# Performance work log

Measured on AMD Instinct MI355X. Metric: run time of the kernel, lower is better.

## Reference

```python
import jax, jax.numpy as jnp
import numpy as np

B, S1, S2 = 32, 60, 60
H, L, D = 100, 20, 300
V, CLS = 30000, 3


def _lstm(x, Wih, Whh, bih, bhh):
    # x: (B,T,Din); PyTorch gate order i,f,g,o
    xp = jnp.einsum('btd,gd->btg', x, Wih) + bih  # (B,T,4H)
    Hh = Whh.shape[1]
    init = (jnp.zeros((x.shape[0], Hh), x.dtype), jnp.zeros((x.shape[0], Hh), x.dtype))
    def step(carry, xt):
        hprev, cprev = carry
        g = xt + hprev @ Whh.T + bhh
        i, f, gg, o = jnp.split(g, 4, axis=-1)
        c = jax.nn.sigmoid(f) * cprev + jax.nn.sigmoid(i) * jnp.tanh(gg)
        hh = jax.nn.sigmoid(o) * jnp.tanh(c)
        return (hh, c), hh
    (hT, _), hs = jax.lax.scan(step, init, jnp.swapaxes(xp, 0, 1))
    return jnp.swapaxes(hs, 0, 1), hT


def _bilstm(x, pf, pb):
    hs_f, hT_f = _lstm(x, *pf)
    hs_b, hT_b = _lstm(x[:, ::-1], *pb)
    return hs_f, hs_b[:, ::-1], hT_f, hT_b


def _mp_single(v1, u, w):
    # cosine(w*v1_i, w*u) per perspective; v1 (B,S,H), u (B,H), w (H,L) -> (B,L,S)
    w2 = w * w
    n1 = jnp.sqrt(jnp.einsum('bih,hl->bil', v1 * v1, w2))
    nu = jnp.sqrt(jnp.einsum('bh,hl->bl', u * u, w2))
    num = jnp.einsum('bih,hl,bh->bil', v1, w2, u)
    return jnp.swapaxes(num / (n1 * nu[:, None, :]), 1, 2)


def _mp_pairwise(v1, v2, w):
    # full (B,L,S1,S2) multi-perspective cosine without materializing (B,L,S,H)
    w2 = w * w
    n1 = jnp.sqrt(jnp.einsum('bih,hl->bil', v1 * v1, w2))  # (B,S1,L)
    n2 = jnp.sqrt(jnp.einsum('bjh,hl->bjl', v2 * v2, w2))  # (B,S2,L)
    num = jnp.einsum('bih,hl,bjh->blij', v1, w2, v2)
    return num / (jnp.moveaxis(n1, 2, 1)[..., None] * jnp.moveaxis(n2, 2, 1)[:, :, None, :])


def _cos_attn(v1, v2):
    n1 = jnp.linalg.norm(v1, axis=2, keepdims=True)
    n2 = jnp.linalg.norm(v2, axis=2, keepdims=True)
    return jnp.einsum('bih,bjh->bij', v1, v2) / (n1 * jnp.swapaxes(n2, 1, 2))


def _match_dir(cp, ch, w_full, w_max, w_am, w_amax, last_idx):
    mv_p_full = _mp_single(cp, ch[:, last_idx], w_full)
    mv_h_full = _mp_single(ch, cp[:, last_idx], w_full)
    m = _mp_pairwise(cp, ch, w_max)
    mv_p_max = m.max(axis=3)
    mv_h_max = m.max(axis=2)
    a = _cos_attn(cp, ch)  # (B,S1,S2)
    mean_h = jnp.einsum('bij,bjh->bih', a, ch) / (a.sum(2, keepdims=True) + 1e-10)
    mean_p = jnp.einsum('bij,bih->bjh', a, cp) / (a.sum(1)[..., None] + 1e-10)
    max_h = (ch[:, None, :, :] * a[..., None]).max(axis=2)  # (B,S1,H)
    max_p = (cp[:, :, None, :] * a[..., None]).max(axis=1)  # (B,S2,H)
    # original code slices [:, :, :, 0] -> matches against v2 position 0
    mv_p_am = _mp_single(cp, mean_h[:, 0], w_am)
    mv_h_am = _mp_single(ch, mean_p[:, 0], w_am)
    mv_p_amax = _mp_single(cp, max_h[:, 0], w_amax)
    mv_h_amax = _mp_single(ch, max_p[:, 0], w_amax)
    return (mv_p_full, mv_p_max, mv_p_am, mv_p_amax), (mv_h_full, mv_h_max, mv_h_am, mv_h_amax)


def _forward(p_idx, h_idx, word_emb, ctxf, ctxb, ws, aggf, aggb, fc1_W, fc1_b, fc2_W, fc2_b):
    p = word_emb[p_idx]
    h = word_emb[h_idx]
    cpf, cpb, _, _ = _bilstm(p, ctxf, ctxb)
    chf, chb, _, _ = _bilstm(h, ctxf, ctxb)
    w1, w2, w3, w4, w5, w6, w7, w8 = ws
    pf, hf = _match_dir(cpf, chf, w1, w3, w5, w7, -1)
    pb, hb = _match_dir(cpb, chb, w2, w4, w6, w8, 0)
    mv_p = jnp.swapaxes(jnp.concatenate(pf + pb, axis=1), 1, 2)  # (B,S1,8L)
    mv_h = jnp.swapaxes(jnp.concatenate(hf + hb, axis=1), 1, 2)
    _, _, pTf, pTb = _bilstm(mv_p, aggf, aggb)
    _, _, hTf, hTb = _bilstm(mv_h, aggf, aggb)
    x = jnp.concatenate([pTf, pTb, hTf, hTb], axis=1)  # (B,4H)
    x = jnp.tanh(x @ fc1_W.T + fc1_b)
    return x @ fc2_W.T + fc2_b


def setup_inputs() -> dict:
    key = jax.random.key(0)
    ks = iter(jax.random.split(key, 48))
    def nrm(shape, s):
        return (jax.random.normal(next(ks), shape) * s).astype(jnp.float32)
    inp = {}
    inp['p'] = jax.random.randint(next(ks), (B, S1), 0, V)
    inp['h'] = jax.random.randint(next(ks), (B, S2), 0, V)
    inp['word_emb'] = nrm((V, D), 0.1)
    for pre, din in (('ctx', D), ('agg', 8 * L)):
        for d in ('f', 'b'):
            inp[pre + '_Wih_' + d] = nrm((4 * H, din), (2.0 / din) ** 0.5)
            inp[pre + '_Whh_' + d] = nrm((4 * H, H), (1.0 / H) ** 0.5)
            inp[pre + '_bih_' + d] = jnp.zeros((4 * H,), jnp.float32)
            inp[pre + '_bhh_' + d] = jnp.zeros((4 * H,), jnp.float32)
    for i in range(1, 9):
        inp['w' + str(i)] = nrm((H, L), (2.0 / H) ** 0.5)
    inp['fc1_W'] = nrm((2 * H, 4 * H), 0.005)
    inp['fc1_b'] = jnp.zeros((2 * H,), jnp.float32)
    inp['fc2_W'] = nrm((CLS, 2 * H), 0.005)
    inp['fc2_b'] = jnp.zeros((CLS,), jnp.float32)
    return inp


def reference(p, h, word_emb, ctx_Wih_f, ctx_Whh_f, ctx_bih_f, ctx_bhh_f, ctx_Wih_b, ctx_Whh_b, ctx_bih_b, ctx_bhh_b, w1, w2, w3, w4, w5, w6, w7, w8, agg_Wih_f, agg_Whh_f, agg_bih_f, agg_bhh_f, agg_Wih_b, agg_Whh_b, agg_bih_b, agg_bhh_b, fc1_W, fc1_b, fc2_W, fc2_b):
    return _forward(p, h, word_emb,
                    (ctx_Wih_f, ctx_Whh_f, ctx_bih_f, ctx_bhh_f),
                    (ctx_Wih_b, ctx_Whh_b, ctx_bih_b, ctx_bhh_b),
                    (w1, w2, w3, w4, w5, w6, w7, w8),
                    (agg_Wih_f, agg_Whh_f, agg_bih_f, agg_bhh_f),
                    (agg_Wih_b, agg_Whh_b, agg_bih_b, agg_bhh_b),
                    fc1_W, fc1_b, fc2_W, fc2_b)
```

## Files before the change

kernel.cpp:

```cpp
#include <hip/hip_runtime.h>
#include <math.h>

#define B_   32
#define T_   60
#define D_   300
#define HID  100
#define G4   400
#define L_   20

#define XP_OFF   0u
#define HSC_OFF  3072000u
#define HSA_OFF  3840000u
#define MV_OFF   4608000u
#define AV_OFF   5222400u

__global__ __launch_bounds__(256) void gemm_dual(
    const float* __restrict__ A0, const float* __restrict__ A1,
    const int* __restrict__ idx0, const int* __restrict__ idx1,
    const float* __restrict__ Wf, const float* __restrict__ Wb,
    const float* __restrict__ bf, const float* __restrict__ bb,
    float* __restrict__ C, int K)
{
    __shared__ float As[16][68];
    __shared__ float Bs[16][68];
    const int tid = threadIdx.x;
    const int m0 = blockIdx.y * 64;
    const int n0 = blockIdx.x * 64;
    const bool is_h = (m0 >= 1920);
    const float* __restrict__ Abase = is_h ? A1 : A0;
    const int* __restrict__ idx = is_h ? idx1 : idx0;
    const int mloc0 = m0 - (is_h ? 1920 : 0);

    const int r = tid >> 2;
    const int q = tid & 3;

    const int arow = mloc0 + r;
    const int srow = idx ? idx[arow] : arow;
    const float* __restrict__ Arow = Abase + (size_t)srow * K;
    const int n_my = n0 + r;
    const float* __restrict__ Wrow = (n_my < 400) ? (Wf + (size_t)n_my * K)
                      : ((n_my < 800) ? (Wb + (size_t)(n_my - 400) * K) : nullptr);

    const int tm = (tid >> 4) << 2;
    const int tn = (tid & 15) << 2;
    float acc[4][4] = {};
    for (int k0 = 0; k0 < K; k0 += 16) {
        const int k = k0 + q * 4;
        float4 av4 = make_float4(0.f, 0.f, 0.f, 0.f);
        float4 bv4 = make_float4(0.f, 0.f, 0.f, 0.f);
        if (k < K) av4 = *reinterpret_cast<const float4*>(Arow + k);
        if (Wrow != nullptr && k < K) bv4 = *reinterpret_cast<const float4*>(Wrow + k);
        __syncthreads();
        As[q * 4 + 0][r] = av4.x; As[q * 4 + 1][r] = av4.y;
        As[q * 4 + 2][r] = av4.z; As[q * 4 + 3][r] = av4.w;
        Bs[q * 4 + 0][r] = bv4.x; Bs[q * 4 + 1][r] = bv4.y;
        Bs[q * 4 + 2][r] = bv4.z; Bs[q * 4 + 3][r] = bv4.w;
        __syncthreads();
        #pragma unroll
        for (int kk = 0; kk < 16; ++kk) {
            const float4 a4 = *reinterpret_cast<const float4*>(&As[kk][tm]);
            const float4 b4 = *reinterpret_cast<const float4*>(&Bs[kk][tn]);
            const float a[4] = {a4.x, a4.y, a4.z, a4.w};
            const float b[4] = {b4.x, b4.y, b4.z, b4.w};
            #pragma unroll
            for (int i = 0; i < 4; i++)
                #pragma unroll
                for (int j = 0; j < 4; j++) acc[i][j] = fmaf(a[i], b[j], acc[i][j]);
        }
    }
    #pragma unroll
    for (int i = 0; i < 4; i++)
        #pragma unroll
        for (int j = 0; j < 4; j++) {
            const int n = n0 + tn + j;
            if (n < 800) {
                const int m = m0 + tm + i;
                const int s = (m >= 1920 ? 2 : 0) + (n >= 400 ? 1 : 0);
                const int ml = m - (m >= 1920 ? 1920 : 0);
                const int nl = n - (n >= 400 ? 400 : 0);
                const float bias = (n >= 400) ? bb[nl] : bf[nl];
                C[((size_t)s * 1920 + ml) * 400 + nl] = acc[i][j] + bias;
            }
        }
}

__global__ __launch_bounds__(512, 1) void lstm_scan(
    const float* __restrict__ xp,
    const float* __restrict__ Whh_f, const float* __restrict__ Whh_b,
    const float* __restrict__ bhh_f, const float* __restrict__ bhh_b,
    float* __restrict__ hs)
{
    const int blk = blockIdx.x;
    const int s = blk >> 5, b = blk & 31;
    const int dir = s & 1;
    const float* __restrict__ Whh = dir ? Whh_b : Whh_f;
    const float* __restrict__ bhh = dir ? bhh_b : bhh_f;
    const int tid = threadIdx.x;

    __shared__ __align__(16) float h_lds[HID];
    __shared__ float gact[G4];

    float wreg[HID];
    float bias = 0.f;
    if (tid < G4) {
        bias = bhh[tid];
        #pragma unroll
        for (int k = 0; k < HID; ++k) wreg[k] = Whh[tid * HID + k];
    }
    if (tid < HID) h_lds[tid] = 0.f;
    float c_reg = 0.f;

    const float* __restrict__ xp0 = xp + ((size_t)s * B_ + b) * T_ * G4;
    float* __restrict__ hs0 = hs + ((size_t)s * B_ + b) * T_ * HID;

    int t = dir ? (T_ - 1) : 0;
    const int tstep = dir ? -1 : 1;
    float xr = (tid < G4) ? xp0[(size_t)t * G4 + tid] : 0.f;
    __syncthreads();

    for (int st = 0; st < T_; ++st) {
        const int tcur = t;
        if (tid < G4) {
            float a0 = bias + xr, a1 = 0.f, a2 = 0.f, a3 = 0.f;
            #pragma unroll
            for (int k = 0; k < HID; k += 4) {
                const float4 h4 = *reinterpret_cast<const float4*>(&h_lds[k]);
                a0 = fmaf(h4.x, wreg[k + 0], a0);
                a1 = fmaf(h4.y, wreg[k + 1], a1);
                a2 = fmaf(h4.z, wreg[k + 2], a2);
                a3 = fmaf(h4.w, wreg[k + 3], a3);
            }
            if (st + 1 < T_) xr = xp0[(size_t)(t + tstep) * G4 + tid];
            const float acc = (a0 + a1) + (a2 + a3);
            const int chunk = tid / HID;
            float av;
            if (chunk == 2) av = tanhf(acc);
            else av = 1.f / (1.f + expf(-acc));
            gact[tid] = av;
        }
        __syncthreads();
        if (tid < HID) {
            const float iv = gact[tid], fv = gact[HID + tid];
            const float gv = gact[2 * HID + tid], ov = gact[3 * HID + tid];
            c_reg = fv * c_reg + iv * gv;
            const float hv = ov * tanhf(c_reg);
            h_lds[tid] = hv;
            hs0[(size_t)tcur * HID + tid] = hv;
        }
        t += tstep;
        __syncthreads();
    }
}

__global__ __launch_bounds__(128) void attn_kernel(
    const float* __restrict__ hs_ctx, float* __restrict__ av)
{
    const int d = blockIdx.x >> 5;
    const int b = blockIdx.x & 31;
    const float* __restrict__ cp = hs_ctx + ((size_t)(0 + d) * B_ + b) * T_ * HID;
    const float* __restrict__ ch = hs_ctx + ((size_t)(2 + d) * B_ + b) * T_ * HID;
    const int tid = threadIdx.x;
    __shared__ float cp0[HID], ch0[HID];
    __shared__ float arow[T_], acol[T_];
    __shared__ float nrm[2], asum[2];
    if (tid < HID) { cp0[tid] = cp[tid]; ch0[tid] = ch[tid]; }
    __syncthreads();
    if (tid < 2) {
        const float* v = tid ? ch0 : cp0;
        float sum = 0.f;
        for (int h = 0; h < HID; h++) sum += v[h] * v[h];
        nrm[tid] = sqrtf(sum);
    }
    __syncthreads();
    if (tid < T_) {
        const float* r = ch + (size_t)tid * HID;
        float dot = 0.f, n2 = 0.f;
        for (int h = 0; h < HID; h++) { const float x = r[h]; dot += cp0[h] * x; n2 += x * x; }
        arow[tid] = dot / (nrm[0] * sqrtf(n2));
    } else if (tid >= 64 && tid < 64 + T_) {
        const int i = tid - 64;
        const float* r = cp + (size_t)i * HID;
        float dot = 0.f, n2 = 0.f;
        for (int h = 0; h < HID; h++) { const float x = r[h]; dot += x * ch0[h]; n2 += x * x; }
        acol[i] = dot / (sqrtf(n2) * nrm[1]);
    }
    __syncthreads();
    if (tid < 2) {
        const float* a = tid ? acol : arow;
        float sum = 0.f;
        for (int j = 0; j < T_; j++) sum += a[j];
        asum[tid] = sum;
    }
    __syncthreads();
    if (tid < HID) {
        float m = 0.f, mx = -INFINITY;
        for (int j = 0; j < T_; j++) {
            const float x = ch[(size_t)j * HID + tid] * arow[j];
            m += x; mx = fmaxf(mx, x);
        }
        av[((size_t)(d * 4 + 0) * B_ + b) * HID + tid] = m / (asum[0] + 1e-10f);
        av[((size_t)(d * 4 + 1) * B_ + b) * HID + tid] = mx;
        float m2 = 0.f, mx2 = -INFINITY;
        for (int i = 0; i < T_; i++) {
            const float x = cp[(size_t)i * HID + tid] * acol[i];
            m2 += x; mx2 = fmaxf(mx2, x);
        }
        av[((size_t)(d * 4 + 2) * B_ + b) * HID + tid] = m2 / (asum[1] + 1e-10f);
        av[((size_t)(d * 4 + 3) * B_ + b) * HID + tid] = mx2;
    }
}

struct MPCfg {
    const float* v1;
    const float* u;
    int ustride;
    const float* w;
    float* outp;
    int choff;
};
struct MPCfgs { MPCfg c[12]; };

__global__ __launch_bounds__(256) void mp_single_kernel(MPCfgs cfgs)
{
    const int ci = blockIdx.x >> 5;
    const int b = blockIdx.x & 31;
    const MPCfg cfg = cfgs.c[ci];
    const int tid = threadIdx.x;
    __shared__ float w2[HID][L_];
    __shared__ float uw[HID][L_];
    __shared__ float u_l[HID];
    __shared__ float nul[L_];
    if (tid < HID) u_l[tid] = cfg.u[(size_t)b * cfg.ustride + tid];
    for (int e = tid; e < HID * L_; e += 256) {
        const float wv = cfg.w[e];
        w2[e / L_][e % L_] = wv * wv;
    }
    __syncthreads();
    for (int e = tid; e < HID * L_; e += 256) uw[e / L_][e % L_] = w2[e / L_][e % L_] * u_l[e / L_];
    if (tid < L_) {
        float sum = 0.f;
        for (int h = 0; h < HID; h++) sum += u_l[h] * u_l[h] * w2[h][tid];
        nul[tid] = sqrtf(sum);
    }
    __syncthreads();
    const float* __restrict__ v1b = cfg.v1 + (size_t)b * T_ * HID;
    for (int p = tid; p < T_ * L_; p += 256) {
        const int i = p / L_, l = p % L_;
        const float* __restrict__ v = v1b + (size_t)i * HID;
        float num = 0.f, den = 0.f;
        for (int h = 0; h < HID; h++) {
            const float x = v[h];
            num = fmaf(x, uw[h][l], num);
            den = fmaf(x * x, w2[h][l], den);
        }
        cfg.outp[((size_t)b * T_ + i) * 160 + cfg.choff + l] = num / (sqrtf(den) * nul[l]);
    }
}

__global__ __launch_bounds__(256) void mp_pair_kernel(
    const float* __restrict__ hs_ctx, const float* __restrict__ w3,
    const float* __restrict__ w4, float* __restrict__ mv_p, float* __restrict__ mv_h)
{
    const int x = blockIdx.x;
    const int l = x % L_;
    const int b = (x / L_) & 31;
    const int d = x / (L_ * B_);
    const float* __restrict__ cp = hs_ctx + ((size_t)(0 + d) * B_ + b) * T_ * HID;
    const float* __restrict__ ch = hs_ctx + ((size_t)(2 + d) * B_ + b) * T_ * HID;
    const float* __restrict__ w = d ? w4 : w3;
    const int tid = threadIdx.x;

    __shared__ __align__(16) float Ut[HID][T_];
    __shared__ __align__(16) float Vt[HID][T_];
    __shared__ float aw[HID];
    __shared__ float rn1[T_], rn2[T_];
    float* pmi = &Ut[0][0];
    float* pmj = &Ut[0][0] + 60 * 17 + 4;

    if (tid < HID) aw[tid] = fabsf(w[tid * L_ + l]);
    __syncthreads();
    for (int e = tid; e < T_ * HID; e += 256) {
        const int i = e / HID, h = e % HID;
        const float a = aw[h];
        Ut[h][i] = cp[e] * a;
        Vt[h][i] = ch[e] * a;
    }
    __syncthreads();
    if (tid < T_) {
        float s = 0.f;
        for (int h = 0; h < HID; h++) { const float v = Ut[h][tid]; s = fmaf(v, v, s); }
        rn1[tid] = 1.0f / sqrtf(s);
    } else if (tid >= 64 && tid < 64 + T_) {
        const int j = tid - 64;
        float s = 0.f;
        for (int h = 0; h < HID; h++) { const float v = Vt[h][j]; s = fmaf(v, v, s); }
        rn2[j] = 1.0f / sqrtf(s);
    }
    __syncthreads();

    float rmax[4], cmax[4];
    int i0 = 0, j0 = 0, ti = 0, tj = 0;
    if (tid < 225) {
        tj = tid % 15;
        ti = tid / 15;
        i0 = tj * 4; j0 = ti * 4;
        float acc[4][4] = {};
        #pragma unroll 4
        for (int h = 0; h < HID; ++h) {
            const float4 u = *reinterpret_cast<const float4*>(&Ut[h][i0]);
            const float4 v = *reinterpret_cast<const float4*>(&Vt[h][j0]);
            const float uu[4] = {u.x, u.y, u.z, u.w};
            const float vv[4] = {v.x, v.y, v.z, v.w};
            #pragma unroll
            for (int r2 = 0; r2 < 4; r2++)
                #pragma unroll
                for (int s2 = 0; s2 < 4; s2++) acc[r2][s2] = fmaf(uu[r2], vv[s2], acc[r2][s2]);
        }
        const float r1[4] = {rn1[i0], rn1[i0 + 1], rn1[i0 + 2], rn1[i0 + 3]};
        const float r2v[4] = {rn2[j0], rn2[j0 + 1], rn2[j0 + 2], rn2[j0 + 3]};
        #pragma unroll
        for (int r2 = 0; r2 < 4; r2++) { rmax[r2] = -INFINITY; }
        #pragma unroll
        for (int s2 = 0; s2 < 4; s2++) { cmax[s2] = -INFINITY; }
        #pragma unroll
        for (int r2 = 0; r2 < 4; r2++)
            #pragma unroll
            for (int s2 = 0; s2 < 4; s2++) {
                const float val = acc[r2][s2] * (r1[r2] * r2v[s2]);
                rmax[r2] = fmaxf(rmax[r2], val);
                cmax[s2] = fmaxf(cmax[s2], val);
            }
    }
    __syncthreads();
    if (tid < 225) {
        #pragma unroll
        for (int r2 = 0; r2 < 4; r2++) pmi[(i0 + r2) * 17 + ti] = rmax[r2];
        #pragma unroll
        for (int s2 = 0; s2 < 4; s2++) pmj[tj * 61 + (j0 + s2)] = cmax[s2];
    }
    __syncthreads();
    if (tid < T_) {
        float mx = -INFINITY;
        for (int q = 0; q < 15; q++) mx = fmaxf(mx, pmi[tid * 17 + q]);
        mv_p[((size_t)b * T_ + tid) * 160 + d * 80 + 20 + l] = mx;
    } else if (tid >= 64 && tid < 64 + T_) {
        const int j = tid - 64;
        float mx = -INFINITY;
        for (int q = 0; q < 15; q++) mx = fmaxf(mx, pmj[q * 61 + j]);
        mv_h[((size_t)b * T_ + j) * 160 + d * 80 + 20 + l] = mx;
    }
}

__global__ __launch_bounds__(256) void fc_final(
    const float* __restrict__ hs_agg, const float* __restrict__ fc1W,
    const float* __restrict__ fc1b, const float* __restrict__ fc2W,
    const float* __restrict__ fc2b, float* __restrict__ out)
{
    const int b = blockIdx.x;
    const int tid = threadIdx.x;
    __shared__ float x[400];
    __shared__ float y[200];
    if (tid < HID) {
        x[tid]           = hs_agg[((size_t)(0 * B_ + b) * T_ + 59) * HID + tid];
        x[HID + tid]     = hs_agg[((size_t)(1 * B_ + b) * T_ + 0) * HID + tid];
        x[2 * HID + tid] = hs_agg[((size_t)(2 * B_ + b) * T_ + 59) * HID + tid];
        x[3 * HID + tid] = hs_agg[((size_t)(3 * B_ + b) * T_ + 0) * HID + tid];
    }
    __syncthreads();
    if (tid < 200) {
        float s = fc1b[tid];
        const float* __restrict__ wr = fc1W + (size_t)tid * 400;
        for (int k = 0; k < 400; k++) s = fmaf(x[k], wr[k], s);
        y[tid] = tanhf(s);
    }
    __syncthreads();
    if (tid < 3) {
        float s = fc2b[tid];
        const float* __restrict__ wr = fc2W + (size_t)tid * 200;
        for (int k = 0; k < 200; k++) s = fmaf(y[k], wr[k], s);
        out[b * 3 + tid] = s;
    }
}

extern "C" void kernel_launch(void* const* d_in, const int* in_sizes, int n_in,
                              void* d_out, int out_size, void* d_ws, size_t ws_size,
                              hipStream_t stream) {
    const int* p_idx = (const int*)d_in[0];
    const int* h_idx = (const int*)d_in[1];
    const float* emb = (const float*)d_in[2];
    const float* ctx_Wih_f = (const float*)d_in[3];
    const float* ctx_Whh_f = (const float*)d_in[4];
    const float* ctx_bih_f = (const float*)d_in[5];
    const float* ctx_bhh_f = (const float*)d_in[6];
    const float* ctx_Wih_b = (const float*)d_in[7];
    const float* ctx_Whh_b = (const float*)d_in[8];
    const float* ctx_bih_b = (const float*)d_in[9];
    const float* ctx_bhh_b = (const float*)d_in[10];
    const float* agg_Wih_f = (const float*)d_in[11];
    const float* agg_Whh_f = (const float*)d_in[12];
    const float* agg_bih_f = (const float*)d_in[13];
    const float* agg_bhh_f = (const float*)d_in[14];
    const float* agg_Wih_b = (const float*)d_in[15];
    const float* agg_Whh_b = (const float*)d_in[16];
    const float* agg_bih_b = (const float*)d_in[17];
    const float* agg_bhh_b = (const float*)d_in[18];
    const float* w1 = (const float*)d_in[19];
    const float* w2 = (const float*)d_in[20];
    const float* w3 = (const float*)d_in[21];
    const float* w4 = (const float*)d_in[22];
    const float* w5 = (const float*)d_in[23];
    const float* w6 = (const float*)d_in[24];
    const float* w7 = (const float*)d_in[25];
    const float* w8 = (const float*)d_in[26];
    const float* fc1W = (const float*)d_in[27];
    const float* fc1b = (const float*)d_in[28];
    const float* fc2W = (const float*)d_in[29];
    const float* fc2b = (const float*)d_in[30];

    float* ws = (float*)d_ws;
    float* xp = ws + XP_OFF;
    float* hsc = ws + HSC_OFF;
    float* hsa = ws + HSA_OFF;
    float* mvp = ws + MV_OFF;
    float* mvh = mvp + (size_t)B_ * T_ * 160;
    float* av = ws + AV_OFF;

    const dim3 ggrid(13, 60);

    gemm_dual<<<ggrid, 256, 0, stream>>>(emb, emb, p_idx, h_idx,
                                         ctx_Wih_f, ctx_Wih_b, ctx_bih_f, ctx_bih_b, xp, 300);

    lstm_scan<<<128, 512, 0, stream>>>(xp, ctx_Whh_f, ctx_Whh_b, ctx_bhh_f, ctx_bhh_b, hsc);

    attn_kernel<<<64, 128, 0, stream>>>(hsc, av);

    MPCfgs cfgs;
    for (int d = 0; d < 2; d++) {
        const float* cp_d = hsc + (size_t)(0 + d) * B_ * T_ * HID;
        const float* ch_d = hsc + (size_t)(2 + d) * B_ * T_ * HID;
        const int last = d ? 0 : (T_ - 1);
        const float* wfull = d ? w2 : w1;
        const float* wam = d ? w6 : w5;
        const float* wamax = d ? w8 : w7;
        float* avp0 = av + (size_t)(d * 4 + 0) * B_ * HID;
        float* avp1 = av + (size_t)(d * 4 + 1) * B_ * HID;
        float* avp2 = av + (size_t)(d * 4 + 2) * B_ * HID;
        float* avp3 = av + (size_t)(d * 4 + 3) * B_ * HID;
        cfgs.c[d * 6 + 0] = {cp_d, ch_d + last * HID, T_ * HID, wfull, mvp, d * 80 + 0};
        cfgs.c[d * 6 + 1] = {cp_d, avp0, HID, wam, mvp, d * 80 + 40};
        cfgs.c[d * 6 + 2] = {cp_d, avp1, HID, wamax, mvp, d * 80 + 60};
        cfgs.c[d * 6 + 3] = {ch_d, cp_d + last * HID, T_ * HID, wfull, mvh, d * 80 + 0};
        cfgs.c[d * 6 + 4] = {ch_d, avp2, HID, wam, mvh, d * 80 + 40};
        cfgs.c[d * 6 + 5] = {ch_d, avp3, HID, wamax, mvh, d * 80 + 60};
    }
    mp_single_kernel<<<384, 256, 0, stream>>>(cfgs);
    mp_pair_kernel<<<1280, 256, 0, stream>>>(hsc, w3, w4, mvp, mvh);

    gemm_dual<<<ggrid, 256, 0, stream>>>(mvp, mvh, nullptr, nullptr,
                                         agg_Wih_f, agg_Wih_b, agg_bih_f, agg_bih_b, xp, 160);

    lstm_scan<<<128, 512, 0, stream>>>(xp, agg_Whh_f, agg_Whh_b, agg_bhh_f, agg_bhh_b, hsa);

    fc_final<<<32, 256, 0, stream>>>(hsa, fc1W, fc1b, fc2W, fc2b, (float*)d_out);
}
```

Measured before the change: 360.6 us.

## Interleave LSTM gates per hidden unit and combine via shuffles, one barrier per step

The input-projection GEMM now writes gate outputs interleaved so the four gates of each hidden unit sit in adjacent lanes. The scan kernel assigns each hidden unit a quad of threads that exchange activations with xor shuffles instead of a shared gate buffer. A double-buffered hidden state removes one of the two barriers per timestep. It also uses a single exp-based activation for both sigmoid and tanh, prefetches the input two steps ahead, and shrinks the block to 448 threads. This cuts per-step synchronisation and LDS traffic on the serial recurrence critical path, at the cost of tighter coupling between the GEMM output layout and the scan.

```diff
diff --git a/kernel.cpp b/kernel.cpp
--- a/kernel.cpp
+++ b/kernel.cpp
@@ -79,12 +79,13 @@
                 const int ml = m - (m >= 1920 ? 1920 : 0);
                 const int nl = n - (n >= 400 ? 400 : 0);
                 const float bias = (n >= 400) ? bb[nl] : bf[nl];
-                C[((size_t)s * 1920 + ml) * 400 + nl] = acc[i][j] + bias;
+                const int pos = (nl % 100) * 4 + nl / 100;
+                C[((size_t)s * 1920 + ml) * 400 + pos] = acc[i][j] + bias;
             }
         }
 }
 
-__global__ __launch_bounds__(512, 1) void lstm_scan(
+__global__ __launch_bounds__(448, 1) void lstm_scan(
     const float* __restrict__ xp,
     const float* __restrict__ Whh_f, const float* __restrict__ Whh_b,
     const float* __restrict__ bhh_f, const float* __restrict__ bhh_b,
@@ -96,18 +97,21 @@
     const float* __restrict__ Whh = dir ? Whh_b : Whh_f;
     const float* __restrict__ bhh = dir ? bhh_b : bhh_f;
     const int tid = threadIdx.x;
-
-    __shared__ __align__(16) float h_lds[HID];
-    __shared__ float gact[G4];
+    const int g = tid & 3;
+    const int j = tid >> 2;
+    const bool act = tid < G4;
+
+    __shared__ __align__(16) float h_lds[2][HID];
 
     float wreg[HID];
     float bias = 0.f;
-    if (tid < G4) {
-        bias = bhh[tid];
-        #pragma unroll
-        for (int k = 0; k < HID; ++k) wreg[k] = Whh[tid * HID + k];
-    }
-    if (tid < HID) h_lds[tid] = 0.f;
+    if (act) {
+        const int row = g * HID + j;
+        bias = bhh[row];
+        #pragma unroll
+        for (int k = 0; k < HID; ++k) wreg[k] = Whh[row * HID + k];
+    }
+    if (tid < HID) h_lds[0][tid] = 0.f;
     float c_reg = 0.f;
 
     const float* __restrict__ xp0 = xp + ((size_t)s * B_ + b) * T_ * G4;
@@ -115,39 +119,44 @@
 
     int t = dir ? (T_ - 1) : 0;
     const int tstep = dir ? -1 : 1;
-    float xr = (tid < G4) ? xp0[(size_t)t * G4 + tid] : 0.f;
+    float xA = 0.f, xB = 0.f;
+    if (act) {
+        xA = xp0[(size_t)t * G4 + tid];
+        xB = xp0[(size_t)(t + tstep) * G4 + tid];
+    }
+    int cur = 0;
     __syncthreads();
 
     for (int st = 0; st < T_; ++st) {
-        const int tcur = t;
-        if (tid < G4) {
-            float a0 = bias + xr, a1 = 0.f, a2 = 0.f, a3 = 0.f;
+        if (act) {
+            const float4* __restrict__ hp = reinterpret_cast<const float4*>(h_lds[cur]);
+            float a0 = bias + xA, a1 = 0.f, a2 = 0.f, a3 = 0.f;
             #pragma unroll
             for (int k = 0; k < HID; k += 4) {
-                const float4 h4 = *reinterpret_cast<const float4*>(&h_lds[k]);
+                const float4 h4 = hp[k >> 2];
                 a0 = fmaf(h4.x, wreg[k + 0], a0);
                 a1 = fmaf(h4.y, wreg[k + 1], a1);
                 a2 = fmaf(h4.z, wreg[k + 2], a2);
                 a3 = fmaf(h4.w, wreg[k + 3], a3);
             }
-            if (st + 1 < T_) xr = xp0[(size_t)(t + tstep) * G4 + tid];
+            xA = xB;
+            if (st + 2 < T_) xB = xp0[(size_t)(t + 2 * tstep) * G4 + tid];
             const float acc = (a0 + a1) + (a2 + a3);
-            const int chunk = tid / HID;
-            float av;
-            if (chunk == 2) av = tanhf(acc);
-            else av = 1.f / (1.f + expf(-acc));
-            gact[tid] = av;
-        }
-        __syncthreads();
-        if (tid < HID) {
-            const float iv = gact[tid], fv = gact[HID + tid];
-            const float gv = gact[2 * HID + tid], ov = gact[3 * HID + tid];
-            c_reg = fv * c_reg + iv * gv;
-            const float hv = ov * tanhf(c_reg);
-            h_lds[tid] = hv;
-            hs0[(size_t)tcur * HID + tid] = hv;
+            const float z = (g == 2) ? (-2.f * acc) : (-acc);
+            const float sig = 1.f / (1.f + expf(z));
+            const float a = (g == 2) ? fmaf(2.f, sig, -1.f) : sig;
+            const float v1 = __shfl_xor(a, 1);
+            const float v2 = __shfl_xor(a, 2);
+            const float v3 = __shfl_xor(v1, 2);
+            if (g == 0) {
+                c_reg = fmaf(v1, c_reg, a * v2);
+                const float hv = v3 * tanhf(c_reg);
+                h_lds[cur ^ 1][j] = hv;
+                hs0[(size_t)t * HID + j] = hv;
+            }
         }
         t += tstep;
+        cur ^= 1;
         __syncthreads();
     }
 }
@@ -430,7 +439,7 @@
     gemm_dual<<<ggrid, 256, 0, stream>>>(emb, emb, p_idx, h_idx,
                                          ctx_Wih_f, ctx_Wih_b, ctx_bih_f, ctx_bih_b, xp, 300);
 
-    lstm_scan<<<128, 512, 0, stream>>>(xp, ctx_Whh_f, ctx_Whh_b, ctx_bhh_f, ctx_bhh_b, hsc);
+    lstm_scan<<<128, 448, 0, stream>>>(xp, ctx_Whh_f, ctx_Whh_b, ctx_bhh_f, ctx_bhh_b, hsc);
 
     attn_kernel<<<64, 128, 0, stream>>>(hsc, av);
 
@@ -459,7 +468,7 @@
     gemm_dual<<<ggrid, 256, 0, stream>>>(mvp, mvh, nullptr, nullptr,
                                          agg_Wih_f, agg_Wih_b, agg_bih_f, agg_bih_b, xp, 160);
 
-    lstm_scan<<<128, 512, 0, stream>>>(xp, agg_Whh_f, agg_Whh_b, agg_bhh_f, agg_bhh_b, hsa);
+    lstm_scan<<<128, 448, 0, stream>>>(xp, agg_Whh_f, agg_Whh_b, agg_bhh_f, agg_bhh_b, hsa);
 
     fc_final<<<32, 256, 0, stream>>>(hsa, fc1W, fc1b, fc2W, fc2b, (float*)d_out);
 }
```

Result: slower. 380.7 us (+5.6%).
